# Performance work log

Measured on AMD Instinct MI355X. Metric: run time of the kernel, lower is better.

The kernel has to match this reference:

```python
import jax, jax.numpy as jnp
import numpy as np

N, E, F_IN, NHID, HEADS, NGRAPHS = 50000, 800000, 128, 256, 4, 16
C = NHID // HEADS          # 64 per-head channels
NEG_SLOPE = 0.2            # PyG GATConv default negative_slope


def setup_inputs() -> dict:
    key = jax.random.key(0)
    k = jax.random.split(key, 7)
    x = jax.random.normal(k[0], (N, F_IN), jnp.float32)
    edge_index = jax.random.randint(k[1], (2, E), 0, N)          # [2, E] src/dst
    batch = jnp.sort(jax.random.randint(k[2], (N,), 0, NGRAPHS))  # node -> graph id
    # learned params of GATConv(F_IN, C, heads=HEADS), concat=True
    W = jax.random.normal(k[3], (F_IN, NHID), jnp.float32) / np.sqrt(F_IN)
    att_src = jax.random.normal(k[4], (HEADS, C), jnp.float32) * 0.1
    att_dst = jax.random.normal(k[5], (HEADS, C), jnp.float32) * 0.1
    bias = jax.random.normal(k[6], (NHID,), jnp.float32) * 0.01
    return {"x": x, "edge_index": edge_index, "batch": batch,
            "W": W, "att_src": att_src, "att_dst": att_dst, "bias": bias}


def _segment_softmax(logits, seg, num_segments):
    # softmax over all edges sharing the same destination node
    m = jax.ops.segment_max(logits, seg, num_segments=num_segments)
    m = jnp.where(jnp.isfinite(m), m, jnp.zeros_like(m))  # guard empty segments
    e = jnp.exp(logits - m[seg])
    s = jax.ops.segment_sum(e, seg, num_segments=num_segments)
    return e / (s[seg] + 1e-16)


def reference(x, edge_index, batch, W, att_src, att_dst, bias):
    n = x.shape[0]
    # PyG GATConv adds self-loops by default
    loops = jnp.arange(n, dtype=edge_index.dtype)
    src = jnp.concatenate([edge_index[0], loops])
    dst = jnp.concatenate([edge_index[1], loops])
    xp = (x @ W).reshape(n, HEADS, C)                       # [N, H, C]
    a_src = jnp.einsum('nhc,hc->nh', xp, att_src)           # [N, H]
    a_dst = jnp.einsum('nhc,hc->nh', xp, att_dst)
    logits = jax.nn.leaky_relu(a_src[src] + a_dst[dst], NEG_SLOPE)  # [E+N, H]
    alpha = _segment_softmax(logits, dst, n)
    msg = xp[src] * alpha[:, :, None]                       # [E+N, H, C]
    out = jax.ops.segment_sum(msg, dst, num_segments=n).reshape(n, NHID) + bias
    h = jax.nn.relu(out)                                    # hidden_act='relu'
    # global max / mean pooling per graph, then concat
    gmax = jax.ops.segment_max(h, batch, num_segments=NGRAPHS)
    cnt = jax.ops.segment_sum(jnp.ones((n, 1), h.dtype), batch, num_segments=NGRAPHS)
    gmean = jax.ops.segment_sum(h, batch, num_segments=NGRAPHS) / (cnt + 1e-16)
    return jnp.concatenate([gmax, gmean], axis=1)           # [NGRAPHS, 2*NHID]
```

## Files before the change

kernel.cpp:

```cpp
#include <hip/hip_runtime.h>

#define NN 50000
#define NE 800000
#define FIN 128
#define NHID 256
#define HEADS 4
#define NG 16
#define ETOT (NE + NN)
#define NEG_SLOPE 0.2f
#define MAXDEG 64

#define NBS ((ETOT + 255) / 256)
#define NBG ((NN + 63) / 64)
#define NPB 128
#define NBP ((NN + NPB - 1) / NPB)
#define ZW (NN + 4096 + 4096 + 1)

__device__ __forceinline__ float lrelu(float x) {
    return x > 0.f ? x : NEG_SLOPE * x;
}
__device__ __forceinline__ unsigned short bf16_rne(float f) {
    unsigned u = __float_as_uint(f);
    unsigned r = (u + 0x7fffu + ((u >> 16) & 1u)) >> 16;
    return (unsigned short)r;
}
__device__ __forceinline__ float bf16_to_f(unsigned short h) {
    return __uint_as_float((unsigned)h << 16);
}
__device__ __forceinline__ float bf16_lo(unsigned u) {
    return __uint_as_float(u << 16);
}
__device__ __forceinline__ float bf16_hi(unsigned u) {
    return __uint_as_float(u & 0xffff0000u);
}

using frag_ab = __attribute__((ext_vector_type(8))) short;
using frag_cd = __attribute__((ext_vector_type(4))) float;

__global__ __launch_bounds__(256) void k_prep(const float* __restrict__ W,
                                              unsigned short* __restrict__ Wt16,
                                              int* __restrict__ zero_base) {
    int bid = blockIdx.x;
    if (bid < 128) {
        int idx = bid * 256 + threadIdx.x;
        int n = idx >> 7;
        int k = idx & 127;
        Wt16[idx] = bf16_rne(W[(size_t)k * NHID + n]);
        return;
    }
    for (int i = (bid - 128) * 256 + threadIdx.x; i < ZW; i += 32 * 256)
        zero_base[i] = 0;
}

__global__ __launch_bounds__(256) void k_main(const float* __restrict__ x,
                                              const unsigned short* __restrict__ Wt16,
                                              const float* __restrict__ att_src,
                                              const float* __restrict__ att_dst,
                                              const int* __restrict__ ei,
                                              int* __restrict__ deg,
                                              unsigned short* __restrict__ elist,
                                              unsigned short* __restrict__ xp16,
                                              float* __restrict__ a_src,
                                              float* __restrict__ a_dst) {
    __shared__ __align__(16) unsigned short smem[64 * 264];
    const int bid = blockIdx.x;
    const int tid = threadIdx.x;

    if (bid >= NBG) {
        int e = (bid - NBG) * 256 + tid;
        if (e >= ETOT) return;
        int s, d;
        if (e < NE) { s = ei[e]; d = ei[NE + e]; } else { s = d = e - NE; }
        int pos = atomicAdd(&deg[d], 1);
        if (pos < MAXDEG) elist[d * MAXDEG + pos] = (unsigned short)s;
        return;
    }

    const int row0 = bid * 64;

    {
        int r = tid >> 2;
        int c0 = (tid & 3) * 32;
        int gr = row0 + r;
        if (gr < NN) {
            #pragma unroll
            for (int i = 0; i < 8; i++) {
                float4 v = *(const float4*)&x[(size_t)gr * FIN + c0 + i * 4];
                ushort4 o;
                o.x = bf16_rne(v.x); o.y = bf16_rne(v.y);
                o.z = bf16_rne(v.z); o.w = bf16_rne(v.w);
                *(ushort4*)&smem[r * 264 + c0 + i * 4] = o;
            }
        } else {
            ushort4 z = {0, 0, 0, 0};
            #pragma unroll
            for (int i = 0; i < 8; i++) *(ushort4*)&smem[r * 264 + c0 + i * 4] = z;
        }
    }
    __syncthreads();

    const int wv = tid >> 6;
    const int lane = tid & 63;
    const int rowhalf = wv >> 1;
    const int colhalf = wv & 1;
    const int m = lane & 15;
    const int q = lane >> 4;
    const int cbase = colhalf * 128;

    frag_cd acc[2][8];
    #pragma unroll
    for (int rt = 0; rt < 2; rt++)
        #pragma unroll
        for (int c = 0; c < 8; c++)
            acc[rt][c] = (frag_cd){0.f, 0.f, 0.f, 0.f};

    #pragma unroll
    for (int k0 = 0; k0 < FIN; k0 += 32) {
        frag_ab af0 = *(const frag_ab*)&smem[(rowhalf * 32 + m) * 264 + k0 + q * 8];
        frag_ab af1 = *(const frag_ab*)&smem[(rowhalf * 32 + 16 + m) * 264 + k0 + q * 8];
        #pragma unroll
        for (int c = 0; c < 8; c++) {
            int n = cbase + c * 16 + m;
            frag_ab bf = *(const frag_ab*)&Wt16[(size_t)n * FIN + k0 + q * 8];
            acc[0][c] = __builtin_amdgcn_mfma_f32_16x16x32_bf16(af0, bf, acc[0][c], 0, 0, 0);
            acc[1][c] = __builtin_amdgcn_mfma_f32_16x16x32_bf16(af1, bf, acc[1][c], 0, 0, 0);
        }
    }

    float asv[8], adv[8];
    #pragma unroll
    for (int c = 0; c < 8; c++) {
        asv[c] = att_src[cbase + c * 16 + m];
        adv[c] = att_dst[cbase + c * 16 + m];
    }
    const int headA = colhalf * 2;
    const int headB = colhalf * 2 + 1;

    #pragma unroll
    for (int rt = 0; rt < 2; rt++) {
        #pragma unroll
        for (int reg = 0; reg < 4; reg++) {
            int grow = row0 + rowhalf * 32 + rt * 16 + q * 4 + reg;
            bool ok = grow < NN;
            float psA = 0.f, psB = 0.f, pdA = 0.f, pdB = 0.f;
            #pragma unroll
            for (int c = 0; c < 4; c++) {
                psA += acc[rt][c][reg] * asv[c];
                pdA += acc[rt][c][reg] * adv[c];
                psB += acc[rt][c + 4][reg] * asv[c + 4];
                pdB += acc[rt][c + 4][reg] * adv[c + 4];
            }
            #pragma unroll
            for (int off = 1; off < 16; off <<= 1) {
                psA += __shfl_xor(psA, off, 64);
                psB += __shfl_xor(psB, off, 64);
                pdA += __shfl_xor(pdA, off, 64);
                pdB += __shfl_xor(pdB, off, 64);
            }
            if (m == 0 && ok) {
                a_src[grow * 4 + headA] = psA;
                a_src[grow * 4 + headB] = psB;
                a_dst[grow * 4 + headA] = pdA;
                a_dst[grow * 4 + headB] = pdB;
            }
        }
    }

    __syncthreads();
    #pragma unroll
    for (int rt = 0; rt < 2; rt++)
        #pragma unroll
        for (int c = 0; c < 8; c++)
            #pragma unroll
            for (int reg = 0; reg < 4; reg++)
                smem[(rowhalf * 32 + rt * 16 + q * 4 + reg) * 264 + cbase + c * 16 + m] =
                    bf16_rne(acc[rt][c][reg]);
    __syncthreads();
    {
        int r = tid >> 2;
        int cg = (tid & 3) * 64;
        int gr = row0 + r;
        if (gr < NN) {
            #pragma unroll
            for (int j = 0; j < 2; j++) {
                uint4 v0 = *(const uint4*)&smem[r * 264 + cg + j * 32];
                uint4 v1 = *(const uint4*)&smem[r * 264 + cg + j * 32 + 8];
                uint4 v2 = *(const uint4*)&smem[r * 264 + cg + j * 32 + 16];
                uint4 v3 = *(const uint4*)&smem[r * 264 + cg + j * 32 + 24];
                *(uint4*)&xp16[(size_t)gr * NHID + cg + j * 32] = v0;
                *(uint4*)&xp16[(size_t)gr * NHID + cg + j * 32 + 8] = v1;
                *(uint4*)&xp16[(size_t)gr * NHID + cg + j * 32 + 16] = v2;
                *(uint4*)&xp16[(size_t)gr * NHID + cg + j * 32 + 24] = v3;
            }
        }
    }
}

__global__ __launch_bounds__(256) void k_agg(const unsigned short* __restrict__ elist,
                                             const int* __restrict__ deg,
                                             const float* __restrict__ a_src,
                                             const float* __restrict__ a_dst,
                                             const unsigned short* __restrict__ xp16,
                                             const float* __restrict__ bias,
                                             unsigned short* __restrict__ hbuf16) {
    __shared__ float wlds[4][MAXDEG][4];
    __shared__ int   slds[4][MAXDEG];
    int wv = threadIdx.x >> 6;
    int lane = threadIdx.x & 63;
    int d = blockIdx.x * 4 + wv;
    if (d >= NN) return;
    int dg = deg[d]; if (dg > MAXDEG) dg = MAXDEG;

    float4 ad = *(const float4*)&a_dst[d * 4];

    float4 w = make_float4(0.f, 0.f, 0.f, 0.f);
    if (lane < dg) {
        int s = elist[d * MAXDEG + lane];
        slds[wv][lane] = s;
        float4 as = *(const float4*)&a_src[s * 4];
        w.x = expf(lrelu(as.x + ad.x));
        w.y = expf(lrelu(as.y + ad.y));
        w.z = expf(lrelu(as.z + ad.z));
        w.w = expf(lrelu(as.w + ad.w));
    }
    *(float4*)&wlds[wv][lane][0] = w;
    float4 sm = w;
    #pragma unroll
    for (int off = 1; off < 64; off <<= 1) {
        sm.x += __shfl_xor(sm.x, off, 64);
        sm.y += __shfl_xor(sm.y, off, 64);
        sm.z += __shfl_xor(sm.z, off, 64);
        sm.w += __shfl_xor(sm.w, off, 64);
    }

    const int half = lane >> 5;
    const int hl = lane & 31;
    const int ch0 = hl * 8;
    const int hh = hl >> 3;
    float denom = (hh == 0 ? sm.x : hh == 1 ? sm.y : hh == 2 ? sm.z : sm.w) + 1e-16f;

    float acc0[8] = {}, acc1[8] = {};
    int e = half;
    for (; e + 2 < dg; e += 4) {
        int sA = slds[wv][e];
        int sB = slds[wv][e + 2];
        float wA = wlds[wv][e][hh];
        float wB = wlds[wv][e + 2][hh];
        uint4 uA = *(const uint4*)&xp16[(size_t)sA * NHID + ch0];
        uint4 uB = *(const uint4*)&xp16[(size_t)sB * NHID + ch0];
        acc0[0] += wA * bf16_lo(uA.x); acc0[1] += wA * bf16_hi(uA.x);
        acc0[2] += wA * bf16_lo(uA.y); acc0[3] += wA * bf16_hi(uA.y);
        acc0[4] += wA * bf16_lo(uA.z); acc0[5] += wA * bf16_hi(uA.z);
        acc0[6] += wA * bf16_lo(uA.w); acc0[7] += wA * bf16_hi(uA.w);
        acc1[0] += wB * bf16_lo(uB.x); acc1[1] += wB * bf16_hi(uB.x);
        acc1[2] += wB * bf16_lo(uB.y); acc1[3] += wB * bf16_hi(uB.y);
        acc1[4] += wB * bf16_lo(uB.z); acc1[5] += wB * bf16_hi(uB.z);
        acc1[6] += wB * bf16_lo(uB.w); acc1[7] += wB * bf16_hi(uB.w);
    }
    if (e < dg) {
        int sA = slds[wv][e];
        float wA = wlds[wv][e][hh];
        uint4 uA = *(const uint4*)&xp16[(size_t)sA * NHID + ch0];
        acc0[0] += wA * bf16_lo(uA.x); acc0[1] += wA * bf16_hi(uA.x);
        acc0[2] += wA * bf16_lo(uA.y); acc0[3] += wA * bf16_hi(uA.y);
        acc0[4] += wA * bf16_lo(uA.z); acc0[5] += wA * bf16_hi(uA.z);
        acc0[6] += wA * bf16_lo(uA.w); acc0[7] += wA * bf16_hi(uA.w);
    }
    #pragma unroll
    for (int j = 0; j < 8; j++) {
        acc0[j] += acc1[j];
        acc0[j] += __shfl_xor(acc0[j], 32, 64);
    }
    if (half == 0) {
        float4 b1 = *(const float4*)&bias[ch0];
        float4 b2 = *(const float4*)&bias[ch0 + 4];
        ushort4 oA, oB;
        oA.x = bf16_rne(fmaxf(acc0[0] / denom + b1.x, 0.f));
        oA.y = bf16_rne(fmaxf(acc0[1] / denom + b1.y, 0.f));
        oA.z = bf16_rne(fmaxf(acc0[2] / denom + b1.z, 0.f));
        oA.w = bf16_rne(fmaxf(acc0[3] / denom + b1.w, 0.f));
        oB.x = bf16_rne(fmaxf(acc0[4] / denom + b2.x, 0.f));
        oB.y = bf16_rne(fmaxf(acc0[5] / denom + b2.y, 0.f));
        oB.z = bf16_rne(fmaxf(acc0[6] / denom + b2.z, 0.f));
        oB.w = bf16_rne(fmaxf(acc0[7] / denom + b2.w, 0.f));
        *(ushort4*)&hbuf16[(size_t)d * NHID + ch0] = oA;
        *(ushort4*)&hbuf16[(size_t)d * NHID + ch0 + 4] = oB;
    }
}

__device__ __forceinline__ int lb_batch(const int* __restrict__ batch, int val) {
    int lo = 0, hi = NN;
    while (lo < hi) {
        int mid = (lo + hi) >> 1;
        if (batch[mid] < val) lo = mid + 1; else hi = mid;
    }
    return lo;
}

__global__ __launch_bounds__(256) void k_poolfinal(const unsigned short* __restrict__ hbuf16,
                                                   const int* __restrict__ batch,
                                                   float* __restrict__ gmax,
                                                   float* __restrict__ gsum,
                                                   int* __restrict__ counter,
                                                   float* __restrict__ out) {
    const int tid = threadIdx.x;
    const int wvv = tid >> 6;
    const int lane = tid & 63;
    const int ch = lane * 4;
    int nA = blockIdx.x * NPB + wvv * 32;
    if (nA < NN) {
        int nB = nA + 32; if (nB > NN) nB = NN;
        float lmax0 = 0.f, lmax1 = 0.f, lmax2 = 0.f, lmax3 = 0.f;
        float lsum0 = 0.f, lsum1 = 0.f, lsum2 = 0.f, lsum3 = 0.f;
        int cur_g = batch[nA];
        for (int n = nA; n < nB; n += 4) {
            int cnt = nB - n; if (cnt > 4) cnt = 4;
            ushort4 v[4]; int gg[4];
            #pragma unroll
            for (int i = 0; i < 4; i++) {
                if (i < cnt) {
                    v[i] = *(const ushort4*)&hbuf16[(size_t)(n + i) * NHID + ch];
                    gg[i] = batch[n + i];
                }
            }
            #pragma unroll
            for (int i = 0; i < 4; i++) {
                if (i < cnt) {
                    if (gg[i] != cur_g) {
                        atomicMax((int*)&gmax[cur_g * NHID + ch + 0], __float_as_int(lmax0));
                        atomicMax((int*)&gmax[cur_g * NHID + ch + 1], __float_as_int(lmax1));
                        atomicMax((int*)&gmax[cur_g * NHID + ch + 2], __float_as_int(lmax2));
                        atomicMax((int*)&gmax[cur_g * NHID + ch + 3], __float_as_int(lmax3));
                        atomicAdd(&gsum[cur_g * NHID + ch + 0], lsum0);
                        atomicAdd(&gsum[cur_g * NHID + ch + 1], lsum1);
                        atomicAdd(&gsum[cur_g * NHID + ch + 2], lsum2);
                        atomicAdd(&gsum[cur_g * NHID + ch + 3], lsum3);
                        lmax0 = lmax1 = lmax2 = lmax3 = 0.f;
                        lsum0 = lsum1 = lsum2 = lsum3 = 0.f;
                        cur_g = gg[i];
                    }
                    float f0 = bf16_to_f(v[i].x), f1 = bf16_to_f(v[i].y);
                    float f2 = bf16_to_f(v[i].z), f3 = bf16_to_f(v[i].w);
                    lmax0 = fmaxf(lmax0, f0); lsum0 += f0;
                    lmax1 = fmaxf(lmax1, f1); lsum1 += f1;
                    lmax2 = fmaxf(lmax2, f2); lsum2 += f2;
                    lmax3 = fmaxf(lmax3, f3); lsum3 += f3;
                }
            }
        }
        atomicMax((int*)&gmax[cur_g * NHID + ch + 0], __float_as_int(lmax0));
        atomicMax((int*)&gmax[cur_g * NHID + ch + 1], __float_as_int(lmax1));
        atomicMax((int*)&gmax[cur_g * NHID + ch + 2], __float_as_int(lmax2));
        atomicMax((int*)&gmax[cur_g * NHID + ch + 3], __float_as_int(lmax3));
        atomicAdd(&gsum[cur_g * NHID + ch + 0], lsum0);
        atomicAdd(&gsum[cur_g * NHID + ch + 1], lsum1);
        atomicAdd(&gsum[cur_g * NHID + ch + 2], lsum2);
        atomicAdd(&gsum[cur_g * NHID + ch + 3], lsum3);
    }

    __shared__ int is_last;
    __threadfence();
    __syncthreads();
    if (tid == 0) {
        int old = atomicAdd(counter, 1);
        is_last = (old == (int)gridDim.x - 1);
    }
    __syncthreads();
    if (!is_last) return;
    __threadfence();

    __shared__ float invc[NG];
    if (tid < NG) {
        int lo = lb_batch(batch, tid);
        int hi = lb_batch(batch, tid + 1);
        invc[tid] = 1.0f / ((float)(hi - lo) + 1e-16f);
    }
    __syncthreads();
    for (int i = tid; i < NG * 512; i += 256) {
        int g = i >> 9;
        int j = i & 511;
        float v;
        if (j < 256) v = __int_as_float(atomicMax((int*)&gmax[g * NHID + j], 0));
        else v = atomicAdd(&gsum[g * NHID + (j - 256)], 0.0f) * invc[g];
        out[i] = v;
    }
}

extern "C" void kernel_launch(void* const* d_in, const int* in_sizes, int n_in,
                              void* d_out, int out_size, void* d_ws, size_t ws_size,
                              hipStream_t stream) {
    const float* x      = (const float*)d_in[0];
    const int*   ei     = (const int*)d_in[1];
    const int*   batch  = (const int*)d_in[2];
    const float* W      = (const float*)d_in[3];
    const float* attS   = (const float*)d_in[4];
    const float* attD   = (const float*)d_in[5];
    const float* bias   = (const float*)d_in[6];
    float* out = (float*)d_out;

    float* ws = (float*)d_ws;
    unsigned short* xp16   = (unsigned short*)ws;
    float*          a_src  = (float*)(xp16 + (size_t)NN * NHID + 256);
    float*          a_dst  = a_src + 200000;
    unsigned short* hbuf16 = (unsigned short*)(a_dst + 200000);
    unsigned short* elist  = hbuf16 + (size_t)NN * NHID;
    int*            deg    = (int*)(elist + (size_t)NN * MAXDEG);
    float*          gmax   = (float*)(deg + NN);
    float*          gsum   = gmax + 4096;
    int*            counter = (int*)(gsum + 4096);
    unsigned short* Wt16   = (unsigned short*)(counter + 1);

    k_prep<<<160, 256, 0, stream>>>(W, Wt16, deg);
    k_main<<<NBG + NBS, 256, 0, stream>>>(x, Wt16, attS, attD, ei, deg, elist,
                                          xp16, a_src, a_dst);
    k_agg<<<(NN + 3) / 4, 256, 0, stream>>>(elist, deg, a_src, a_dst, xp16, bias, hbuf16);
    k_poolfinal<<<NBP, 256, 0, stream>>>(hbuf16, batch, gmax, gsum, counter, out);
}
```

Baseline: 260.0 us.

## Store projected features in channel-sliced layout and aggregate per slice for cache locality

The GEMM epilogue now writes xp in 8 channel slices of 32 bf16 values each, laid out [slice][node][32], in place of row-major [node][256]. The aggregation kernel assigns each block one slice, so consecutive blocks gather from a 3.2MB slice that is more likely to stay in L2/MALL. Each wave handles 4 destinations with 8 edge groups of 8 lanes. Softmax weights and edge indices are recomputed per slice, and the 64-byte gathers are narrower, so edge-list reads and exp work grow eightfold.

```diff
diff --git a/kernel.cpp b/kernel.cpp
--- a/kernel.cpp
+++ b/kernel.cpp
@@ -14,6 +14,7 @@
 #define NBG ((NN + 63) / 64)
 #define NPB 128
 #define NBP ((NN + NPB - 1) / NPB)
+#define NBA (8 * ((NN + 15) / 16))
 #define ZW (NN + 4096 + 4096 + 1)
 
 __device__ __forceinline__ float lrelu(float x) {
@@ -59,7 +60,7 @@
                                               const int* __restrict__ ei,
                                               int* __restrict__ deg,
                                               unsigned short* __restrict__ elist,
-                                              unsigned short* __restrict__ xp16,
+                                              unsigned short* __restrict__ xp16s,
                                               float* __restrict__ a_src,
                                               float* __restrict__ a_dst) {
     __shared__ __align__(16) unsigned short smem[64 * 264];
@@ -179,19 +180,23 @@
     {
         int r = tid >> 2;
         int cg = (tid & 3) * 64;
+        int s0 = (tid & 3) * 2;
         int gr = row0 + r;
         if (gr < NN) {
-            #pragma unroll
-            for (int j = 0; j < 2; j++) {
-                uint4 v0 = *(const uint4*)&smem[r * 264 + cg + j * 32];
-                uint4 v1 = *(const uint4*)&smem[r * 264 + cg + j * 32 + 8];
-                uint4 v2 = *(const uint4*)&smem[r * 264 + cg + j * 32 + 16];
-                uint4 v3 = *(const uint4*)&smem[r * 264 + cg + j * 32 + 24];
-                *(uint4*)&xp16[(size_t)gr * NHID + cg + j * 32] = v0;
-                *(uint4*)&xp16[(size_t)gr * NHID + cg + j * 32 + 8] = v1;
-                *(uint4*)&xp16[(size_t)gr * NHID + cg + j * 32 + 16] = v2;
-                *(uint4*)&xp16[(size_t)gr * NHID + cg + j * 32 + 24] = v3;
-            }
+            uint4 v0 = *(const uint4*)&smem[r * 264 + cg];
+            uint4 v1 = *(const uint4*)&smem[r * 264 + cg + 8];
+            uint4 v2 = *(const uint4*)&smem[r * 264 + cg + 16];
+            uint4 v3 = *(const uint4*)&smem[r * 264 + cg + 24];
+            uint4 v4 = *(const uint4*)&smem[r * 264 + cg + 32];
+            uint4 v5 = *(const uint4*)&smem[r * 264 + cg + 40];
+            uint4 v6 = *(const uint4*)&smem[r * 264 + cg + 48];
+            uint4 v7 = *(const uint4*)&smem[r * 264 + cg + 56];
+            unsigned short* p0 = &xp16s[((size_t)s0 * NN + gr) * 32];
+            unsigned short* p1 = &xp16s[((size_t)(s0 + 1) * NN + gr) * 32];
+            *(uint4*)&p0[0] = v0;  *(uint4*)&p0[8] = v1;
+            *(uint4*)&p0[16] = v2; *(uint4*)&p0[24] = v3;
+            *(uint4*)&p1[0] = v4;  *(uint4*)&p1[8] = v5;
+            *(uint4*)&p1[16] = v6; *(uint4*)&p1[24] = v7;
         }
     }
 }
@@ -200,91 +205,57 @@
                                              const int* __restrict__ deg,
                                              const float* __restrict__ a_src,
                                              const float* __restrict__ a_dst,
-                                             const unsigned short* __restrict__ xp16,
+                                             const unsigned short* __restrict__ xp16s,
                                              const float* __restrict__ bias,
                                              unsigned short* __restrict__ hbuf16) {
-    __shared__ float wlds[4][MAXDEG][4];
-    __shared__ int   slds[4][MAXDEG];
-    int wv = threadIdx.x >> 6;
-    int lane = threadIdx.x & 63;
-    int d = blockIdx.x * 4 + wv;
-    if (d >= NN) return;
-    int dg = deg[d]; if (dg > MAXDEG) dg = MAXDEG;
-
-    float4 ad = *(const float4*)&a_dst[d * 4];
-
-    float4 w = make_float4(0.f, 0.f, 0.f, 0.f);
-    if (lane < dg) {
-        int s = elist[d * MAXDEG + lane];
-        slds[wv][lane] = s;
-        float4 as = *(const float4*)&a_src[s * 4];
-        w.x = expf(lrelu(as.x + ad.x));
-        w.y = expf(lrelu(as.y + ad.y));
-        w.z = expf(lrelu(as.z + ad.z));
-        w.w = expf(lrelu(as.w + ad.w));
-    }
-    *(float4*)&wlds[wv][lane][0] = w;
-    float4 sm = w;
-    #pragma unroll
-    for (int off = 1; off < 64; off <<= 1) {
-        sm.x += __shfl_xor(sm.x, off, 64);
-        sm.y += __shfl_xor(sm.y, off, 64);
-        sm.z += __shfl_xor(sm.z, off, 64);
-        sm.w += __shfl_xor(sm.w, off, 64);
-    }
-
-    const int half = lane >> 5;
-    const int hl = lane & 31;
-    const int ch0 = hl * 8;
-    const int hh = hl >> 3;
-    float denom = (hh == 0 ? sm.x : hh == 1 ? sm.y : hh == 2 ? sm.z : sm.w) + 1e-16f;
-
-    float acc0[8] = {}, acc1[8] = {};
-    int e = half;
-    for (; e + 2 < dg; e += 4) {
-        int sA = slds[wv][e];
-        int sB = slds[wv][e + 2];
-        float wA = wlds[wv][e][hh];
-        float wB = wlds[wv][e + 2][hh];
-        uint4 uA = *(const uint4*)&xp16[(size_t)sA * NHID + ch0];
-        uint4 uB = *(const uint4*)&xp16[(size_t)sB * NHID + ch0];
-        acc0[0] += wA * bf16_lo(uA.x); acc0[1] += wA * bf16_hi(uA.x);
-        acc0[2] += wA * bf16_lo(uA.y); acc0[3] += wA * bf16_hi(uA.y);
-        acc0[4] += wA * bf16_lo(uA.z); acc0[5] += wA * bf16_hi(uA.z);
-        acc0[6] += wA * bf16_lo(uA.w); acc0[7] += wA * bf16_hi(uA.w);
-        acc1[0] += wB * bf16_lo(uB.x); acc1[1] += wB * bf16_hi(uB.x);
-        acc1[2] += wB * bf16_lo(uB.y); acc1[3] += wB * bf16_hi(uB.y);
-        acc1[4] += wB * bf16_lo(uB.z); acc1[5] += wB * bf16_hi(uB.z);
-        acc1[6] += wB * bf16_lo(uB.w); acc1[7] += wB * bf16_hi(uB.w);
-    }
-    if (e < dg) {
-        int sA = slds[wv][e];
-        float wA = wlds[wv][e][hh];
-        uint4 uA = *(const uint4*)&xp16[(size_t)sA * NHID + ch0];
-        acc0[0] += wA * bf16_lo(uA.x); acc0[1] += wA * bf16_hi(uA.x);
-        acc0[2] += wA * bf16_lo(uA.y); acc0[3] += wA * bf16_hi(uA.y);
-        acc0[4] += wA * bf16_lo(uA.z); acc0[5] += wA * bf16_hi(uA.z);
-        acc0[6] += wA * bf16_lo(uA.w); acc0[7] += wA * bf16_hi(uA.w);
-    }
-    #pragma unroll
-    for (int j = 0; j < 8; j++) {
-        acc0[j] += acc1[j];
-        acc0[j] += __shfl_xor(acc0[j], 32, 64);
-    }
-    if (half == 0) {
-        float4 b1 = *(const float4*)&bias[ch0];
-        float4 b2 = *(const float4*)&bias[ch0 + 4];
-        ushort4 oA, oB;
-        oA.x = bf16_rne(fmaxf(acc0[0] / denom + b1.x, 0.f));
-        oA.y = bf16_rne(fmaxf(acc0[1] / denom + b1.y, 0.f));
-        oA.z = bf16_rne(fmaxf(acc0[2] / denom + b1.z, 0.f));
-        oA.w = bf16_rne(fmaxf(acc0[3] / denom + b1.w, 0.f));
-        oB.x = bf16_rne(fmaxf(acc0[4] / denom + b2.x, 0.f));
-        oB.y = bf16_rne(fmaxf(acc0[5] / denom + b2.y, 0.f));
-        oB.z = bf16_rne(fmaxf(acc0[6] / denom + b2.z, 0.f));
-        oB.w = bf16_rne(fmaxf(acc0[7] / denom + b2.w, 0.f));
-        *(ushort4*)&hbuf16[(size_t)d * NHID + ch0] = oA;
-        *(ushort4*)&hbuf16[(size_t)d * NHID + ch0 + 4] = oB;
+    const int s = blockIdx.x & 7;
+    const int chunk = blockIdx.x >> 3;
+    const int wv = threadIdx.x >> 6;
+    const int lane = threadIdx.x & 63;
+    const int g = lane >> 3;
+    const int ll = lane & 7;
+    const int h = s >> 1;
+    const int ch = s * 32 + ll * 4;
+
+    const unsigned short* slice_base = &xp16s[(size_t)s * NN * 32];
+    float4 b4 = *(const float4*)&bias[ch];
+
+    int d0 = chunk * 16 + wv * 4;
+    #pragma unroll
+    for (int di = 0; di < 4; di++) {
+        int d = d0 + di;
+        if (d >= NN) break;
+        int dg = deg[d]; if (dg > MAXDEG) dg = MAXDEG;
+        float ad = a_dst[d * 4 + h];
+
+        float a0 = 0.f, a1 = 0.f, a2 = 0.f, a3 = 0.f, wsum = 0.f;
+        for (int e = g; e < dg; e += 8) {
+            int src = elist[d * MAXDEG + e];
+            float w = expf(lrelu(a_src[src * 4 + h] + ad));
+            wsum += w;
+            uint2 u = *(const uint2*)&slice_base[(size_t)src * 32 + ll * 4];
+            a0 += w * bf16_lo(u.x);
+            a1 += w * bf16_hi(u.x);
+            a2 += w * bf16_lo(u.y);
+            a3 += w * bf16_hi(u.y);
+        }
+        #pragma unroll
+        for (int off = 8; off < 64; off <<= 1) {
+            wsum += __shfl_xor(wsum, off, 64);
+            a0 += __shfl_xor(a0, off, 64);
+            a1 += __shfl_xor(a1, off, 64);
+            a2 += __shfl_xor(a2, off, 64);
+            a3 += __shfl_xor(a3, off, 64);
+        }
+        if (g == 0) {
+            float inv = 1.0f / (wsum + 1e-16f);
+            ushort4 o;
+            o.x = bf16_rne(fmaxf(a0 * inv + b4.x, 0.f));
+            o.y = bf16_rne(fmaxf(a1 * inv + b4.y, 0.f));
+            o.z = bf16_rne(fmaxf(a2 * inv + b4.z, 0.f));
+            o.w = bf16_rne(fmaxf(a3 * inv + b4.w, 0.f));
+            *(ushort4*)&hbuf16[(size_t)d * NHID + ch] = o;
+        }
     }
 }
 
@@ -399,8 +370,8 @@
     float* out = (float*)d_out;
 
     float* ws = (float*)d_ws;
-    unsigned short* xp16   = (unsigned short*)ws;
-    float*          a_src  = (float*)(xp16 + (size_t)NN * NHID + 256);
+    unsigned short* xp16s  = (unsigned short*)ws;
+    float*          a_src  = (float*)(xp16s + (size_t)NN * NHID + 256);
     float*          a_dst  = a_src + 200000;
     unsigned short* hbuf16 = (unsigned short*)(a_dst + 200000);
     unsigned short* elist  = hbuf16 + (size_t)NN * NHID;
@@ -412,7 +383,7 @@
 
     k_prep<<<160, 256, 0, stream>>>(W, Wt16, deg);
     k_main<<<NBG + NBS, 256, 0, stream>>>(x, Wt16, attS, attD, ei, deg, elist,
-                                          xp16, a_src, a_dst);
-    k_agg<<<(NN + 3) / 4, 256, 0, stream>>>(elist, deg, a_src, a_dst, xp16, bias, hbuf16);
+                                          xp16s, a_src, a_dst);
+    k_agg<<<NBA, 256, 0, stream>>>(elist, deg, a_src, a_dst, xp16s, bias, hbuf16);
     k_poolfinal<<<NBP, 256, 0, stream>>>(hbuf16, batch, gmax, gsum, counter, out);
 }
```

New measurement: 341.7 us. 31.4% more time.

## Handle self-loops implicitly in aggregation and batch 4 edges per thread in scatter

Applied to the files above, without the earlier changes.

Self-loop edges are no longer inserted into the per-destination edge list through atomics. The aggregation kernel now computes the self-loop weight directly from a_src/a_dst of the node and adds its message after the reduction, which removes N atomics and frees one MAXDEG slot per node. The edge-scatter path also processes four edges per thread so more loads and atomics are in flight at once. The cost is extra per-node loads and exp work in k_agg, plus a changed overflow semantic: the self-loop no longer counts toward MAXDEG.

```diff
diff --git a/kernel.cpp b/kernel.cpp
--- a/kernel.cpp
+++ b/kernel.cpp
@@ -10,8 +10,8 @@
 #define NEG_SLOPE 0.2f
 #define MAXDEG 64
 
-#define NBS ((ETOT + 255) / 256)
 #define NBG ((NN + 63) / 64)
+#define NBS ((NE + 1023) / 1024)
 #define NPB 128
 #define NBP ((NN + NPB - 1) / NPB)
 #define ZW (NN + 4096 + 4096 + 1)
@@ -67,12 +67,22 @@
     const int tid = threadIdx.x;
 
     if (bid >= NBG) {
-        int e = (bid - NBG) * 256 + tid;
-        if (e >= ETOT) return;
-        int s, d;
-        if (e < NE) { s = ei[e]; d = ei[NE + e]; } else { s = d = e - NE; }
-        int pos = atomicAdd(&deg[d], 1);
-        if (pos < MAXDEG) elist[d * MAXDEG + pos] = (unsigned short)s;
+        int base = (bid - NBG) * 1024 + tid;
+        int e0 = base, e1 = base + 256, e2 = base + 512, e3 = base + 768;
+        int s0 = 0, s1 = 0, s2 = 0, s3 = 0, d0 = -1, d1 = -1, d2 = -1, d3 = -1;
+        if (e0 < NE) { s0 = ei[e0]; d0 = ei[NE + e0]; }
+        if (e1 < NE) { s1 = ei[e1]; d1 = ei[NE + e1]; }
+        if (e2 < NE) { s2 = ei[e2]; d2 = ei[NE + e2]; }
+        if (e3 < NE) { s3 = ei[e3]; d3 = ei[NE + e3]; }
+        int p0 = -1, p1 = -1, p2 = -1, p3 = -1;
+        if (d0 >= 0) p0 = atomicAdd(&deg[d0], 1);
+        if (d1 >= 0) p1 = atomicAdd(&deg[d1], 1);
+        if (d2 >= 0) p2 = atomicAdd(&deg[d2], 1);
+        if (d3 >= 0) p3 = atomicAdd(&deg[d3], 1);
+        if (p0 >= 0 && p0 < MAXDEG) elist[d0 * MAXDEG + p0] = (unsigned short)s0;
+        if (p1 >= 0 && p1 < MAXDEG) elist[d1 * MAXDEG + p1] = (unsigned short)s1;
+        if (p2 >= 0 && p2 < MAXDEG) elist[d2 * MAXDEG + p2] = (unsigned short)s2;
+        if (p3 >= 0 && p3 < MAXDEG) elist[d3 * MAXDEG + p3] = (unsigned short)s3;
         return;
     }
 
@@ -212,6 +222,12 @@
     int dg = deg[d]; if (dg > MAXDEG) dg = MAXDEG;
 
     float4 ad = *(const float4*)&a_dst[d * 4];
+    float4 asd = *(const float4*)&a_src[d * 4];
+    float4 wself;
+    wself.x = expf(lrelu(asd.x + ad.x));
+    wself.y = expf(lrelu(asd.y + ad.y));
+    wself.z = expf(lrelu(asd.z + ad.z));
+    wself.w = expf(lrelu(asd.w + ad.w));
 
     float4 w = make_float4(0.f, 0.f, 0.f, 0.f);
     if (lane < dg) {
@@ -237,7 +253,8 @@
     const int hl = lane & 31;
     const int ch0 = hl * 8;
     const int hh = hl >> 3;
-    float denom = (hh == 0 ? sm.x : hh == 1 ? sm.y : hh == 2 ? sm.z : sm.w) + 1e-16f;
+    float wsv = (hh == 0 ? wself.x : hh == 1 ? wself.y : hh == 2 ? wself.z : wself.w);
+    float denom = (hh == 0 ? sm.x : hh == 1 ? sm.y : hh == 2 ? sm.z : sm.w) + wsv + 1e-16f;
 
     float acc0[8] = {}, acc1[8] = {};
     int e = half;
@@ -272,6 +289,12 @@
         acc0[j] += __shfl_xor(acc0[j], 32, 64);
     }
     if (half == 0) {
+        uint4 us = *(const uint4*)&xp16[(size_t)d * NHID + ch0];
+        acc0[0] += wsv * bf16_lo(us.x); acc0[1] += wsv * bf16_hi(us.x);
+        acc0[2] += wsv * bf16_lo(us.y); acc0[3] += wsv * bf16_hi(us.y);
+        acc0[4] += wsv * bf16_lo(us.z); acc0[5] += wsv * bf16_hi(us.z);
+        acc0[6] += wsv * bf16_lo(us.w); acc0[7] += wsv * bf16_hi(us.w);
+
         float4 b1 = *(const float4*)&bias[ch0];
         float4 b2 = *(const float4*)&bias[ch0 + 4];
         ushort4 oA, oB;
```

Measured after the change: 269.3 us. +3.6%, slower.
